# Kernel tuning notes

Hardware: AMD Instinct MI355X
Metric: run time of the kernel (lower is better)

Reference implementation:

```python
import jax, jax.numpy as jnp
import numpy as np

N = 4096
D = 256          # hidden_dim
H = 8            # num_heads
HD = D // H      # head_dim
EPS = 1e-5
SCALE = D ** -0.5  # note: full hidden_dim, as in the torch code


def setup_inputs() -> dict:
    key = jax.random.key(0)
    ks = jax.random.split(key, 12)
    # binary-ish adjacency mask in [0,1); zeros/near-zeros act like masked entries
    A = (jax.random.uniform(ks[0], (N, N)) < 0.01).astype(jnp.float32)
    h = jax.random.normal(ks[1], (N, D), dtype=jnp.float32)
    s = D ** -0.5
    Wq = jax.random.normal(ks[2], (D, D), dtype=jnp.float32) * s
    Wk = jax.random.normal(ks[3], (D, D), dtype=jnp.float32) * s
    Wv = jax.random.normal(ks[4], (D, D), dtype=jnp.float32) * s
    Wo = jax.random.normal(ks[5], (D, D), dtype=jnp.float32) * s
    g1 = jnp.ones((D,), jnp.float32)
    b1 = jnp.zeros((D,), jnp.float32)
    g2 = jnp.ones((D,), jnp.float32)
    b2 = jnp.zeros((D,), jnp.float32)
    W1 = jax.random.normal(ks[6], (2 * D, D), dtype=jnp.float32) * s
    W2 = jax.random.normal(ks[7], (D, 2 * D), dtype=jnp.float32) * (2 * D) ** -0.5
    return {"A": A, "h": h, "Wq": Wq, "Wk": Wk, "Wv": Wv, "Wo": Wo,
            "g1": g1, "b1": b1, "g2": g2, "b2": b2, "W1": W1, "W2": W2}


def _batchnorm(x, g, b):
    # training-mode BatchNorm1d over node/batch dim, biased variance
    m = x.mean(axis=0)
    v = x.var(axis=0)
    return (x - m) * jax.lax.rsqrt(v + EPS) * g + b


def _mha(A, h, Wq, Wk, Wv, Wo):
    # torch reshape(N, head_dim, num_heads): head index is the fastest axis
    q = (h @ Wq.T).reshape(N, HD, H) * SCALE   # [N, hd, H]
    k = (h @ Wk.T).reshape(N, HD, H)
    v = (h @ Wv.T).reshape(N, HD, H)
    scores = jnp.einsum('ndh,mdh->hnm', q, k)  # [H, N, N]
    attn = jax.nn.softmax(A[None, :, :] * scores, axis=2)
    out = jnp.einsum('hnm,mdh->ndh', attn, v)  # [N, hd, H]
    return out.reshape(N, D) @ Wo.T


def reference(A, h, Wq, Wk, Wv, Wo, g1, b1, g2, b2, W1, W2):
    h1 = h
    h = _mha(A, h, Wq, Wk, Wv, Wo)
    h = h + h1                       # residual
    h = _batchnorm(h, g1, b1)
    h2 = h
    h = jax.nn.relu(h @ W1.T) @ W2.T  # FFN (no bias)
    h = h2 + h                       # residual
    h = _batchnorm(h, g2, b2)
    return h
```

## Files before the change

kernel.cpp:

```cpp
#include <hip/hip_runtime.h>
#include <math.h>

#define NN 4096
#define DIM 256
#define NHEAD 8
#define HDIM 32
#define DFF 512
#define CAP 128
#define EPS_BN 1e-5f
#define QSCALE 0.0625f
#define MB (1u << 20)

typedef __attribute__((ext_vector_type(8))) short short8;
typedef __attribute__((ext_vector_type(4))) float f32x4;

__device__ inline ushort f2bf(float x) {
    unsigned u = __builtin_bit_cast(unsigned, x);
    unsigned r = u + 0x7FFF + ((u >> 16) & 1);
    return (ushort)(r >> 16);
}
__device__ inline float bf2f(ushort u) {
    return __builtin_bit_cast(float, (unsigned)u << 16);
}
__device__ inline float bflo(unsigned u) { return __builtin_bit_cast(float, u << 16); }
__device__ inline float bfhi(unsigned u) { return __builtin_bit_cast(float, u & 0xFFFF0000u); }

__global__ __launch_bounds__(256) void convert_bf(
    const float* __restrict__ s0, const float* __restrict__ s1,
    const float* __restrict__ s2, const float* __restrict__ s3,
    const float* __restrict__ s4, const float* __restrict__ s5,
    const float* __restrict__ s6,
    ushort* d0, ushort* d1, ushort* d2, ushort* d3,
    ushort* d4, ushort* d5, ushort* d6)
{
    int b = blockIdx.x, tid = threadIdx.x;
    const float* s; ushort* d; int off;
    if      (b < 512) { s = s0; d = d0; off = b; }
    else if (b < 544) { s = s1; d = d1; off = b - 512; }
    else if (b < 576) { s = s2; d = d2; off = b - 544; }
    else if (b < 608) { s = s3; d = d3; off = b - 576; }
    else if (b < 640) { s = s4; d = d4; off = b - 608; }
    else if (b < 704) { s = s5; d = d5; off = b - 640; }
    else              { s = s6; d = d6; off = b - 704; }
    size_t base = (size_t)off * 2048 + (size_t)tid * 8;
    float4 f0 = *(const float4*)(s + base);
    float4 f1 = *(const float4*)(s + base + 4);
    uint4 u;
    u.x = (unsigned)f2bf(f0.x) | ((unsigned)f2bf(f0.y) << 16);
    u.y = (unsigned)f2bf(f0.z) | ((unsigned)f2bf(f0.w) << 16);
    u.z = (unsigned)f2bf(f1.x) | ((unsigned)f2bf(f1.y) << 16);
    u.w = (unsigned)f2bf(f1.z) | ((unsigned)f2bf(f1.w) << 16);
    *(uint4*)(d + base) = u;
}

#define LDP 88
#define TSTRIDE 74
__global__ __launch_bounds__(256) void qkv_ascan(
    const ushort* __restrict__ Ah, const ushort* __restrict__ B,
    ushort* __restrict__ qh, ushort* __restrict__ kvh,
    float* __restrict__ vpart,
    const float* __restrict__ Araw, unsigned* __restrict__ packed,
    int* __restrict__ cnt)
{
    __shared__ ushort As[64][LDP];
    __shared__ ushort Bs[64][LDP];
    __shared__ float sRedS[8][64];
    int b = blockIdx.x, tid = threadIdx.x;

    if (b >= 768) {
        int* scan = (int*)&As[0][0];
        int n = b - 768;
        const float* row = Araw + (size_t)n * NN;
        float4 vals[4];
        int c = 0;
        #pragma unroll
        for (int i = 0; i < 4; ++i) {
            vals[i] = *(const float4*)(row + i * 1024 + tid * 4);
            c += (vals[i].x != 0.f) + (vals[i].y != 0.f)
               + (vals[i].z != 0.f) + (vals[i].w != 0.f);
        }
        scan[tid] = c;
        __syncthreads();
        for (int off = 1; off < 256; off <<= 1) {
            int t = (tid >= off) ? scan[tid - off] : 0;
            __syncthreads();
            scan[tid] += t;
            __syncthreads();
        }
        int pos = scan[tid] - c;
        int total = scan[255];
        #pragma unroll
        for (int i = 0; i < 4; ++i) {
            int cb = i * 1024 + tid * 4;
            float4 v = vals[i];
            if (v.x != 0.f && pos < CAP) { packed[n*CAP+pos] = ((unsigned)f2bf(v.x) << 16) | (unsigned)cb;       ++pos; }
            if (v.y != 0.f && pos < CAP) { packed[n*CAP+pos] = ((unsigned)f2bf(v.y) << 16) | (unsigned)(cb + 1); ++pos; }
            if (v.z != 0.f && pos < CAP) { packed[n*CAP+pos] = ((unsigned)f2bf(v.z) << 16) | (unsigned)(cb + 2); ++pos; }
            if (v.w != 0.f && pos < CAP) { packed[n*CAP+pos] = ((unsigned)f2bf(v.w) << 16) | (unsigned)(cb + 3); ++pos; }
        }
        if (tid == 0) cnt[n] = min(total, CAP);
        return;
    }

    int lane = tid & 63, w = tid >> 6;
    int wm = (w >> 1) * 32, wn = (w & 1) * 32;
    int xcd = b & 7, pos = b >> 3;
    int by = xcd * 8 + pos / 12;
    int bx = pos % 12;
    int m0 = by * 64, n0 = bx * 64;
    int l15 = lane & 15, lk = lane >> 4;
    int srow = tid >> 3;
    int scol = (tid & 7) * 8;

    f32x4 acc[2][2] = {};
    for (int k0 = 0; k0 < DIM; k0 += 64) {
        const ushort* Bg = B + (size_t)(n0 + srow) * DIM + scol + k0;
        uint4 gb0 = *(const uint4*)Bg;
        uint4 gb1 = *(const uint4*)(Bg + (size_t)32 * DIM);
        const ushort* Ag = Ah + (size_t)(m0 + srow) * DIM + scol + k0;
        uint4 ga0 = *(const uint4*)Ag;
        uint4 ga1 = *(const uint4*)(Ag + (size_t)32 * DIM);
        __syncthreads();
        *(uint4*)&As[srow][scol]      = ga0;
        *(uint4*)&As[srow + 32][scol] = ga1;
        *(uint4*)&Bs[srow][scol]      = gb0;
        *(uint4*)&Bs[srow + 32][scol] = gb1;
        __syncthreads();
        #pragma unroll
        for (int ks = 0; ks < 2; ++ks) {
            int kc = ks * 32 + lk * 8;
            short8 a0 = *(const short8*)&As[wm      + l15][kc];
            short8 a1 = *(const short8*)&As[wm + 16 + l15][kc];
            short8 b0 = *(const short8*)&Bs[wn      + l15][kc];
            short8 b1 = *(const short8*)&Bs[wn + 16 + l15][kc];
            acc[0][0] = __builtin_amdgcn_mfma_f32_16x16x32_bf16(a0, b0, acc[0][0], 0, 0, 0);
            acc[0][1] = __builtin_amdgcn_mfma_f32_16x16x32_bf16(a0, b1, acc[0][1], 0, 0, 0);
            acc[1][0] = __builtin_amdgcn_mfma_f32_16x16x32_bf16(a1, b0, acc[1][0], 0, 0, 0);
            acc[1][1] = __builtin_amdgcn_mfma_f32_16x16x32_bf16(a1, b1, acc[1][1], 0, 0, 0);
        }
    }
    ushort* sT = &As[0][0];
    int seg = n0 >> 8, ddBase = (n0 & 255) >> 3;
    float sp[2] = {0.f, 0.f};
    __syncthreads();
    #pragma unroll
    for (int mt = 0; mt < 2; ++mt)
        #pragma unroll
        for (int nt = 0; nt < 2; ++nt) {
            int col_l = wn + nt * 16 + l15;
            #pragma unroll
            for (int i = 0; i < 4; ++i) {
                int row_l = wm + mt * 16 + lk * 4 + i;
                float v = acc[mt][nt][i];
                if (seg == 0) v *= QSCALE;
                sT[row_l * TSTRIDE + col_l] = f2bf(v);
                sp[nt] += v;
            }
        }
    __syncthreads();
    for (int c = tid; c < 512; c += 256) {
        int rl = c & 63, hh = c >> 6;
        const ushort* tp = sT + rl * TSTRIDE + hh;
        uint4 pk;
        pk.x = (unsigned)tp[0]  | ((unsigned)tp[8]  << 16);
        pk.y = (unsigned)tp[16] | ((unsigned)tp[24] << 16);
        pk.z = (unsigned)tp[32] | ((unsigned)tp[40] << 16);
        pk.w = (unsigned)tp[48] | ((unsigned)tp[56] << 16);
        int row = m0 + rl;
        if (seg == 0)
            *(uint4*)(qh + ((size_t)hh * NN + row) * HDIM + ddBase) = pk;
        else
            *(uint4*)(kvh + ((size_t)hh * NN + row) * 64 +
                      ((seg == 2) ? 32 : 0) + ddBase) = pk;
    }
    if (seg == 2) {
        int slot = ((wm >> 5) << 2) | lk;
        sRedS[slot][wn + l15]      = sp[0];
        sRedS[slot][wn + 16 + l15] = sp[1];
        __syncthreads();
        if (tid < 64) {
            float ss = 0.f;
            #pragma unroll
            for (int r = 0; r < 8; ++r) ss += sRedS[r][tid];
            vpart[(size_t)by * 256 + (n0 & 255) + tid] = ss;
        }
    }
}

__global__ __launch_bounds__(256) void gemm_bf(
    const void* __restrict__ Aptr, const ushort* __restrict__ B,
    const float* __restrict__ scA, const float* __restrict__ shA,
    const float* __restrict__ resid,
    const float* yres, const float* __restrict__ scR, const float* __restrict__ shR,
    float* Cf, ushort* __restrict__ Cb,
    float* __restrict__ bnps, float* __restrict__ bnpq,
    int M, int Nn, int K, int aMode, int storeMode, int relu, int bnstat)
{
    __shared__ ushort As[64][LDP];
    __shared__ ushort Bs[64][LDP];
    __shared__ float sRedS[8][64];
    __shared__ float sRedQ[8][64];
    int tid = threadIdx.x;
    int lane = tid & 63, w = tid >> 6;
    int wm = (w >> 1) * 32, wn = (w & 1) * 32;
    int nbx = gridDim.x, nbyq = gridDim.y >> 3;
    int orig = blockIdx.y * nbx + blockIdx.x;
    int xcd = orig & 7, pos = orig >> 3;
    int by = xcd * nbyq + pos / nbx;
    int bx = pos % nbx;
    int m0 = by * 64, n0 = bx * 64;
    int l15 = lane & 15, lk = lane >> 4;
    int srow = tid >> 3;
    int scol = (tid & 7) * 8;

    f32x4 acc[2][2] = {};
    for (int k0 = 0; k0 < K; k0 += 64) {
        uint4 ga0, ga1, gb0, gb1;
        const ushort* Bg = B + (size_t)(n0 + srow) * K + scol + k0;
        gb0 = *(const uint4*)Bg;
        gb1 = *(const uint4*)(Bg + (size_t)32 * K);
        if (aMode == 0) {
            const ushort* Ag = (const ushort*)Aptr + (size_t)(m0 + srow) * K + scol + k0;
            ga0 = *(const uint4*)Ag;
            ga1 = *(const uint4*)(Ag + (size_t)32 * K);
        } else {
            const float* Af = (const float*)Aptr + (size_t)(m0 + srow) * K + scol + k0;
            float4 sc0 = *(const float4*)(scA + k0 + scol);
            float4 sc1 = *(const float4*)(scA + k0 + scol + 4);
            float4 sh0 = *(const float4*)(shA + k0 + scol);
            float4 sh1 = *(const float4*)(shA + k0 + scol + 4);
            float4 a0 = *(const float4*)Af;
            float4 a1 = *(const float4*)(Af + 4);
            float4 b0 = *(const float4*)(Af + (size_t)32 * K);
            float4 b1 = *(const float4*)(Af + (size_t)32 * K + 4);
            ga0.x = (unsigned)f2bf(a0.x*sc0.x+sh0.x) | ((unsigned)f2bf(a0.y*sc0.y+sh0.y) << 16);
            ga0.y = (unsigned)f2bf(a0.z*sc0.z+sh0.z) | ((unsigned)f2bf(a0.w*sc0.w+sh0.w) << 16);
            ga0.z = (unsigned)f2bf(a1.x*sc1.x+sh1.x) | ((unsigned)f2bf(a1.y*sc1.y+sh1.y) << 16);
            ga0.w = (unsigned)f2bf(a1.z*sc1.z+sh1.z) | ((unsigned)f2bf(a1.w*sc1.w+sh1.w) << 16);
            ga1.x = (unsigned)f2bf(b0.x*sc0.x+sh0.x) | ((unsigned)f2bf(b0.y*sc0.y+sh0.y) << 16);
            ga1.y = (unsigned)f2bf(b0.z*sc0.z+sh0.z) | ((unsigned)f2bf(b0.w*sc0.w+sh0.w) << 16);
            ga1.z = (unsigned)f2bf(b1.x*sc1.x+sh1.x) | ((unsigned)f2bf(b1.y*sc1.y+sh1.y) << 16);
            ga1.w = (unsigned)f2bf(b1.z*sc1.z+sh1.z) | ((unsigned)f2bf(b1.w*sc1.w+sh1.w) << 16);
        }
        __syncthreads();
        *(uint4*)&As[srow][scol]      = ga0;
        *(uint4*)&As[srow + 32][scol] = ga1;
        *(uint4*)&Bs[srow][scol]      = gb0;
        *(uint4*)&Bs[srow + 32][scol] = gb1;
        __syncthreads();
        #pragma unroll
        for (int ks = 0; ks < 2; ++ks) {
            int kc = ks * 32 + lk * 8;
            short8 a0 = *(const short8*)&As[wm      + l15][kc];
            short8 a1 = *(const short8*)&As[wm + 16 + l15][kc];
            short8 b0 = *(const short8*)&Bs[wn      + l15][kc];
            short8 b1 = *(const short8*)&Bs[wn + 16 + l15][kc];
            acc[0][0] = __builtin_amdgcn_mfma_f32_16x16x32_bf16(a0, b0, acc[0][0], 0, 0, 0);
            acc[0][1] = __builtin_amdgcn_mfma_f32_16x16x32_bf16(a0, b1, acc[0][1], 0, 0, 0);
            acc[1][0] = __builtin_amdgcn_mfma_f32_16x16x32_bf16(a1, b0, acc[1][0], 0, 0, 0);
            acc[1][1] = __builtin_amdgcn_mfma_f32_16x16x32_bf16(a1, b1, acc[1][1], 0, 0, 0);
        }
    }

    float sp[2] = {0.f, 0.f}, qp[2] = {0.f, 0.f};
    #pragma unroll
    for (int mt = 0; mt < 2; ++mt) {
        #pragma unroll
        for (int nt = 0; nt < 2; ++nt) {
            int col = n0 + wn + nt * 16 + l15;
            #pragma unroll
            for (int i = 0; i < 4; ++i) {
                int row = m0 + wm + mt * 16 + lk * 4 + i;
                float v = acc[mt][nt][i];
                if (storeMode == 0) {
                    if (resid) v += resid[(size_t)row * Nn + col];
                    Cf[(size_t)row * Nn + col] = v;
                } else if (storeMode == 1) {
                    if (relu) v = fmaxf(v, 0.f);
                    Cb[(size_t)row * Nn + col] = f2bf(v);
                } else {
                    v += yres[(size_t)row * Nn + col] * scR[col] + shR[col];
                    Cf[(size_t)row * Nn + col] = v;
                }
                if (bnstat) { sp[nt] += v; qp[nt] += v * v; }
            }
        }
    }
    if (bnstat) {
        int slot = ((wm >> 5) << 2) | lk;
        sRedS[slot][wn + l15]      = sp[0];
        sRedQ[slot][wn + l15]      = qp[0];
        sRedS[slot][wn + 16 + l15] = sp[1];
        sRedQ[slot][wn + 16 + l15] = qp[1];
        __syncthreads();
        if (tid < 64) {
            float ss = 0.f, qq = 0.f;
            #pragma unroll
            for (int r = 0; r < 8; ++r) { ss += sRedS[r][tid]; qq += sRedQ[r][tid]; }
            bnps[(size_t)by * DIM + n0 + tid] = ss;
            bnpq[(size_t)by * DIM + n0 + tid] = qq;
        }
    }
}

__global__ __launch_bounds__(256) void vsum_final(
    const float* __restrict__ vpart, float* __restrict__ vsumh)
{
    int c = threadIdx.x;
    float s = 0.f;
    #pragma unroll 8
    for (int b = 0; b < 64; ++b) s += vpart[(size_t)b * 256 + c];
    vsumh[(c & 7) * HDIM + (c >> 3)] = s;
}

__global__ __launch_bounds__(1024) void colreduce_final2(
    const float* __restrict__ ps, const float* __restrict__ pq,
    const float* __restrict__ g, const float* __restrict__ bsh,
    float* __restrict__ scale, float* __restrict__ shift)
{
    __shared__ float rs_[4][256], rq_[4][256];
    int t = threadIdx.x;
    int c = t & 255, qd = t >> 8;
    float s = 0.f, q = 0.f;
    for (int b = qd; b < 64; b += 4) {
        s += ps[b * DIM + c];
        q += pq[b * DIM + c];
    }
    rs_[qd][c] = s; rq_[qd][c] = q;
    __syncthreads();
    if (qd == 0) {
        s = rs_[0][c] + rs_[1][c] + rs_[2][c] + rs_[3][c];
        q = rq_[0][c] + rq_[1][c] + rq_[2][c] + rq_[3][c];
        float m = s * (1.f / NN);
        float var = q * (1.f / NN) - m * m;
        float rstd = rsqrtf(var + EPS_BN);
        float sc = rstd * g[c];
        scale[c] = sc;
        shift[c] = bsh[c] - m * sc;
    }
}

__global__ __launch_bounds__(256) void bn_apply_fin(
    const float* __restrict__ x, const float* __restrict__ scale,
    const float* __restrict__ shift, float* __restrict__ out)
{
    int tid = threadIdx.x;
    size_t i = (size_t)blockIdx.x * 1024 + (size_t)tid * 4;
    int c = (tid * 4) & 255;
    float4 v = *(const float4*)(x + i);
    float4 sc = *(const float4*)(scale + c);
    float4 sh = *(const float4*)(shift + c);
    float4 r;
    r.x = v.x * sc.x + sh.x;
    r.y = v.y * sc.y + sh.y;
    r.z = v.z * sc.z + sh.z;
    r.w = v.w * sc.w + sh.w;
    *(float4*)(out + i) = r;
}

__global__ __launch_bounds__(256) void attn3(
    const ushort* __restrict__ qh, const ushort* __restrict__ kvh,
    const float* __restrict__ vsumh,
    const unsigned* __restrict__ packed, const int* __restrict__ cnt,
    ushort* __restrict__ out)
{
    __shared__ float    sQ[8][32];
    __shared__ unsigned sPk[8][CAP];
    __shared__ float    sS[8][CAP];
    __shared__ float    sRd[8];

    int tid = threadIdx.x, b = blockIdx.x;
    int hH = b & 7, rg = b >> 3;
    int r = tid >> 5, l = tid & 31;
    int n = rg * 8 + r;
    int nnz = cnt[n];

    sQ[r][l] = bf2f(qh[((size_t)hH * NN + n) * HDIM + l]);
    for (int j = l; j < nnz; j += 32) sPk[r][j] = packed[n * CAP + j];
    __syncthreads();

    float4 qreg[8];
    #pragma unroll
    for (int t = 0; t < 8; ++t) qreg[t] = ((const float4*)sQ[r])[t];
    float lsum = 0.0f;
    for (int j = l; j < nnz; j += 32) {
        unsigned pk = sPk[r][j];
        int m = pk & 0xFFFF;
        float a = bfhi(pk);
        const uint4* kp = (const uint4*)(kvh + ((size_t)hH * NN + m) * 64);
        uint4 k0 = kp[0], k1 = kp[1], k2 = kp[2], k3 = kp[3];
        float s =
            bflo(k0.x)*qreg[0].x + bfhi(k0.x)*qreg[0].y +
            bflo(k0.y)*qreg[0].z + bfhi(k0.y)*qreg[0].w +
            bflo(k0.z)*qreg[1].x + bfhi(k0.z)*qreg[1].y +
            bflo(k0.w)*qreg[1].z + bfhi(k0.w)*qreg[1].w +
            bflo(k1.x)*qreg[2].x + bfhi(k1.x)*qreg[2].y +
            bflo(k1.y)*qreg[2].z + bfhi(k1.y)*qreg[2].w +
            bflo(k1.z)*qreg[3].x + bfhi(k1.z)*qreg[3].y +
            bflo(k1.w)*qreg[3].z + bfhi(k1.w)*qreg[3].w +
            bflo(k2.x)*qreg[4].x + bfhi(k2.x)*qreg[4].y +
            bflo(k2.y)*qreg[4].z + bfhi(k2.y)*qreg[4].w +
            bflo(k2.z)*qreg[5].x + bfhi(k2.z)*qreg[5].y +
            bflo(k2.w)*qreg[5].z + bfhi(k2.w)*qreg[5].w +
            bflo(k3.x)*qreg[6].x + bfhi(k3.x)*qreg[6].y +
            bflo(k3.y)*qreg[6].z + bfhi(k3.y)*qreg[6].w +
            bflo(k3.z)*qreg[7].x + bfhi(k3.z)*qreg[7].y +
            bflo(k3.w)*qreg[7].z + bfhi(k3.w)*qreg[7].w;
        s *= a;
        float ww = __expf(s);
        sS[r][j] = ww - 1.0f;
        lsum += ww;
    }
    #pragma unroll
    for (int o = 16; o > 0; o >>= 1) lsum += __shfl_xor(lsum, o, 32);
    if (l == 0) sRd[r] = 1.0f / (lsum + (float)(NN - nnz));
    __syncthreads();

    const ushort* vbase = kvh + (size_t)hH * NN * 64 + 32 + l;
    float acc = 0.f;
    #pragma unroll 4
    for (int j = 0; j < nnz; ++j) {
        int m = sPk[r][j] & 0xFFFF;
        acc += sS[r][j] * bf2f(vbase[(size_t)m * 64]);
    }
    float res = (acc + vsumh[hH * HDIM + l]) * sRd[r];
    out[(size_t)n * DIM + l * 8 + hH] = f2bf(res);
}

extern "C" void kernel_launch(void* const* d_in, const int* in_sizes, int n_in,
                              void* d_out, int out_size, void* d_ws, size_t ws_size,
                              hipStream_t stream)
{
    const float* A  = (const float*)d_in[0];
    const float* h  = (const float*)d_in[1];
    const float* Wq = (const float*)d_in[2];
    const float* Wk = (const float*)d_in[3];
    const float* Wv = (const float*)d_in[4];
    const float* Wo = (const float*)d_in[5];
    const float* g1 = (const float*)d_in[6];
    const float* b1 = (const float*)d_in[7];
    const float* g2 = (const float*)d_in[8];
    const float* b2 = (const float*)d_in[9];
    const float* W1 = (const float*)d_in[10];
    const float* W2 = (const float*)d_in[11];
    float* out = (float*)d_out;
    char* w = (char*)d_ws;

    unsigned* packed = (unsigned*)(w);
    int*    nzcnt  = (int*)(w + 2 * MB);
    ushort* h_bf   = (ushort*)(w + 3 * MB);
    ushort* wqkv   = (ushort*)(w + 5 * MB);
    ushort* wo_b   = (ushort*)(w + 5 * MB + 384 * 1024);
    ushort* w1_b   = (ushort*)(w + 5 * MB + 512 * 1024);
    ushort* w2_b   = (ushort*)(w + 5 * MB + 768 * 1024);
    ushort* qh_bf  = (ushort*)(w + 6 * MB);
    ushort* kvh    = (ushort*)(w + 8 * MB);
    ushort* ao_bf  = (ushort*)(w + 12 * MB);
    float*  y      = (float*)(w + 14 * MB);
    ushort* t_bf   = (ushort*)(w + 18 * MB);
    float*  vpart  = (float*)(w + 22 * MB);
    float*  bnps   = (float*)(w + 23 * MB);
    float*  bnpq   = (float*)(w + 23 * MB + 64 * 1024);
    float*  scale1 = (float*)(w + 24 * MB);
    float*  shift1 = scale1 + 256;
    float*  scale2 = scale1 + 512;
    float*  shift2 = scale1 + 768;
    float*  vsumh  = scale1 + 1024;

    dim3 blk(256);

    convert_bf<<<768, blk, 0, stream>>>(h, Wq, Wk, Wv, Wo, W1, W2,
        h_bf, wqkv, wqkv + 65536, wqkv + 131072, wo_b, w1_b, w2_b);
    qkv_ascan<<<4864, blk, 0, stream>>>(h_bf, wqkv, qh_bf, kvh, vpart,
                                        A, packed, nzcnt);
    vsum_final<<<1, blk, 0, stream>>>(vpart, vsumh);
    attn3<<<NN, blk, 0, stream>>>(qh_bf, kvh, vsumh, packed, nzcnt, ao_bf);
    gemm_bf<<<dim3(4, 64), blk, 0, stream>>>(ao_bf, wo_b,
        nullptr, nullptr, h, nullptr, nullptr, nullptr,
        y, nullptr, bnps, bnpq, NN, DIM, DIM, 0, 0, 0, 1);
    colreduce_final2<<<1, dim3(1024), 0, stream>>>(bnps, bnpq, g1, b1, scale1, shift1);
    gemm_bf<<<dim3(8, 64), blk, 0, stream>>>(y, w1_b,
        scale1, shift1, nullptr, nullptr, nullptr, nullptr,
        nullptr, t_bf, nullptr, nullptr, NN, DFF, DIM, 1, 1, 1, 0);
    gemm_bf<<<dim3(4, 64), blk, 0, stream>>>(t_bf, w2_b,
        nullptr, nullptr, nullptr, y, scale1, shift1,
        y, nullptr, bnps, bnpq, NN, DIM, DFF, 0, 3, 0, 1);
    colreduce_final2<<<1, dim3(1024), 0, stream>>>(bnps, bnpq, g2, b2, scale2, shift2);
    bn_apply_fin<<<1024, blk, 0, stream>>>(y, scale2, shift2, out);
}
```

Before: 100.3 us.

## Store attention output head-major and vectorize sparse V accumulation

The attention kernel now writes its output in a head-major [H][N][32] layout with packed 8-byte stores, in place of scattered 2-byte writes at stride 8. The Wo weight columns are permuted during conversion to match, and the Wo GEMM gets a new A-load mode that reads the head-major layout. The V accumulation loop is split across 4 nonzero subsets per row, with each lane loading 4 bf16 values at once and a shuffle reduction at the end. The goal is fewer, wider memory transactions, at the cost of extra shuffles and a strided gather in the weight conversion.

```diff
diff --git a/kernel.cpp b/kernel.cpp
--- a/kernel.cpp
+++ b/kernel.cpp
@@ -34,12 +34,27 @@
     ushort* d4, ushort* d5, ushort* d6)
 {
     int b = blockIdx.x, tid = threadIdx.x;
+    if (b >= 608 && b < 640) {
+        int off = b - 608;
+        int row = off * 8 + (tid >> 5), t = tid & 31;
+        int hh = t >> 2, dd0 = (t & 3) * 8;
+        const float* src = s4 + (size_t)row * 256 + hh;
+        ushort tmp[8];
+        #pragma unroll
+        for (int i = 0; i < 8; ++i) tmp[i] = f2bf(src[(size_t)(dd0 + i) * 8]);
+        uint4 u;
+        u.x = (unsigned)tmp[0] | ((unsigned)tmp[1] << 16);
+        u.y = (unsigned)tmp[2] | ((unsigned)tmp[3] << 16);
+        u.z = (unsigned)tmp[4] | ((unsigned)tmp[5] << 16);
+        u.w = (unsigned)tmp[6] | ((unsigned)tmp[7] << 16);
+        *(uint4*)(d4 + (size_t)row * 256 + hh * 32 + dd0) = u;
+        return;
+    }
     const float* s; ushort* d; int off;
     if      (b < 512) { s = s0; d = d0; off = b; }
     else if (b < 544) { s = s1; d = d1; off = b - 512; }
     else if (b < 576) { s = s2; d = d2; off = b - 544; }
     else if (b < 608) { s = s3; d = d3; off = b - 576; }
-    else if (b < 640) { s = s4; d = d4; off = b - 608; }
     else if (b < 704) { s = s5; d = d5; off = b - 640; }
     else              { s = s6; d = d6; off = b - 704; }
     size_t base = (size_t)off * 2048 + (size_t)tid * 8;
@@ -223,6 +238,13 @@
             const ushort* Ag = (const ushort*)Aptr + (size_t)(m0 + srow) * K + scol + k0;
             ga0 = *(const uint4*)Ag;
             ga1 = *(const uint4*)(Ag + (size_t)32 * K);
+        } else if (aMode == 2) {
+            int c0 = k0 + scol;
+            int hh = c0 >> 5, dd = c0 & 31;
+            const ushort* Ag = (const ushort*)Aptr +
+                ((size_t)hh * NN + m0 + srow) * HDIM + dd;
+            ga0 = *(const uint4*)Ag;
+            ga1 = *(const uint4*)(Ag + (size_t)32 * HDIM);
         } else {
             const float* Af = (const float*)Aptr + (size_t)(m0 + srow) * K + scol + k0;
             float4 sc0 = *(const float4*)(scA + k0 + scol);
@@ -362,7 +384,7 @@
     const ushort* __restrict__ qh, const ushort* __restrict__ kvh,
     const float* __restrict__ vsumh,
     const unsigned* __restrict__ packed, const int* __restrict__ cnt,
-    ushort* __restrict__ out)
+    ushort* __restrict__ outh)
 {
     __shared__ float    sQ[8][32];
     __shared__ unsigned sPk[8][CAP];
@@ -416,15 +438,36 @@
     if (l == 0) sRd[r] = 1.0f / (lsum + (float)(NN - nnz));
     __syncthreads();
 
-    const ushort* vbase = kvh + (size_t)hH * NN * 64 + 32 + l;
-    float acc = 0.f;
-    #pragma unroll 4
-    for (int j = 0; j < nnz; ++j) {
+    int jsub = l >> 3, dq = l & 7;
+    const ushort* vbase = kvh + (size_t)hH * NN * 64 + 32 + dq * 4;
+    float a0 = 0.f, a1 = 0.f, a2 = 0.f, a3 = 0.f;
+    for (int j = jsub; j < nnz; j += 4) {
+        float ww = sS[r][j];
         int m = sPk[r][j] & 0xFFFF;
-        acc += sS[r][j] * bf2f(vbase[(size_t)m * 64]);
-    }
-    float res = (acc + vsumh[hH * HDIM + l]) * sRd[r];
-    out[(size_t)n * DIM + l * 8 + hH] = f2bf(res);
+        uint2 vv = *(const uint2*)(vbase + (size_t)m * 64);
+        a0 += ww * bflo(vv.x); a1 += ww * bfhi(vv.x);
+        a2 += ww * bflo(vv.y); a3 += ww * bfhi(vv.y);
+    }
+    #pragma unroll
+    for (int o = 8; o < 32; o <<= 1) {
+        a0 += __shfl_xor(a0, o, 32);
+        a1 += __shfl_xor(a1, o, 32);
+        a2 += __shfl_xor(a2, o, 32);
+        a3 += __shfl_xor(a3, o, 32);
+    }
+    if (jsub == 0) {
+        float rd = sRd[r];
+        int d0 = dq * 4;
+        const float* vs = vsumh + hH * HDIM + d0;
+        float r0 = (a0 + vs[0]) * rd;
+        float r1 = (a1 + vs[1]) * rd;
+        float r2 = (a2 + vs[2]) * rd;
+        float r3 = (a3 + vs[3]) * rd;
+        uint2 st;
+        st.x = (unsigned)f2bf(r0) | ((unsigned)f2bf(r1) << 16);
+        st.y = (unsigned)f2bf(r2) | ((unsigned)f2bf(r3) << 16);
+        *(uint2*)(outh + ((size_t)hH * NN + n) * HDIM + d0) = st;
+    }
 }
 
 extern "C" void kernel_launch(void* const* d_in, const int* in_sizes, int n_in,
@@ -455,7 +498,7 @@
     ushort* w2_b   = (ushort*)(w + 5 * MB + 768 * 1024);
     ushort* qh_bf  = (ushort*)(w + 6 * MB);
     ushort* kvh    = (ushort*)(w + 8 * MB);
-    ushort* ao_bf  = (ushort*)(w + 12 * MB);
+    ushort* ao_hb  = (ushort*)(w + 12 * MB);
     float*  y      = (float*)(w + 14 * MB);
     ushort* t_bf   = (ushort*)(w + 18 * MB);
     float*  vpart  = (float*)(w + 22 * MB);
@@ -474,10 +517,10 @@
     qkv_ascan<<<4864, blk, 0, stream>>>(h_bf, wqkv, qh_bf, kvh, vpart,
                                         A, packed, nzcnt);
     vsum_final<<<1, blk, 0, stream>>>(vpart, vsumh);
-    attn3<<<NN, blk, 0, stream>>>(qh_bf, kvh, vsumh, packed, nzcnt, ao_bf);
-    gemm_bf<<<dim3(4, 64), blk, 0, stream>>>(ao_bf, wo_b,
+    attn3<<<NN, blk, 0, stream>>>(qh_bf, kvh, vsumh, packed, nzcnt, ao_hb);
+    gemm_bf<<<dim3(4, 64), blk, 0, stream>>>(ao_hb, wo_b,
         nullptr, nullptr, h, nullptr, nullptr, nullptr,
-        y, nullptr, bnps, bnpq, NN, DIM, DIM, 0, 0, 0, 1);
+        y, nullptr, bnps, bnpq, NN, DIM, DIM, 2, 0, 0, 1);
     colreduce_final2<<<1, dim3(1024), 0, stream>>>(bnps, bnpq, g1, b1, scale1, shift1);
     gemm_bf<<<dim3(8, 64), blk, 0, stream>>>(y, w1_b,
         scale1, shift1, nullptr, nullptr, nullptr, nullptr,
```

Measured after the change: 94.94 us. -5.3%, faster.
